# Kernel optimization log

Measured on AMD Instinct MI355X. Metric: run time of the kernel, lower is better.

Reference implementation:

```python
import jax, jax.numpy as jnp
import numpy as np

EPS_LN = 1e-6
EPS_NORM = 1e-7


def conv1x1(x, w, b):
    # x: [B,Cin,H,W], w: [Cout,Cin], b: [Cout]
    return jnp.einsum('bchw,oc->bohw', x, w) + b[None, :, None, None]


def ln2d(x, g, beta):
    u = x.mean(1, keepdims=True)
    s = ((x - u) ** 2).mean(1, keepdims=True)
    return g[None, :, None, None] * ((x - u) / jnp.sqrt(s + EPS_LN)) + beta[None, :, None, None]


def gather_neighborhoods(x, r):
    # x: [B,C,H,W] -> [B,C,n,H,W] with zero padding, n=(2r+1)**2
    B, C, H, W = x.shape
    xp = jnp.pad(x, ((0, 0), (0, 0), (r, r), (r, r)))
    slices = [xp[:, :, dy:dy + H, dx:dx + W]
              for dy in range(2 * r + 1) for dx in range(2 * r + 1)]
    return jnp.stack(slices, axis=2)


def valid_mask(H, W, r):
    offs = jnp.arange(-r, r + 1)
    hh = jnp.arange(H)
    ww = jnp.arange(W)
    vy = ((hh[None, :] + offs[:, None]) >= 0) & ((hh[None, :] + offs[:, None]) < H)  # [d,H]
    vx = ((ww[None, :] + offs[:, None]) >= 0) & ((ww[None, :] + offs[:, None]) < W)  # [d,W]
    return (vy[:, None, :, None] & vx[None, :, None, :]).reshape((2 * r + 1) ** 2, H, W)


def setup_inputs() -> dict:
    key = jax.random.key(0)
    B, C, H, W, r = 2, 64, 112, 112, 3
    n2 = (2 * r + 1) ** 2  # 49
    ks = jax.random.split(key, 16)
    s = 0.02
    inp = {
        'spatial_feats': jax.random.normal(ks[0], (B, C, H, W), jnp.float32),
        'semantic_feats': jax.random.normal(ks[1], (B, C, H, W), jnp.float32),
        # range_proj: conv1x1 -> LN2d -> SiLU -> conv1x1
        'rp_w1': s * jax.random.normal(ks[2], (C, C), jnp.float32), 'rp_b1': jnp.zeros((C,), jnp.float32),
        'rp_g': jnp.ones((C,), jnp.float32), 'rp_beta': jnp.zeros((C,), jnp.float32),
        'rp_w2': s * jax.random.normal(ks[3], (C, C), jnp.float32), 'rp_b2': jnp.zeros((C,), jnp.float32),
        # fixup_proj: conv1x1 (n2+C -> n2) -> LN2d -> SiLU -> conv1x1 (n2->n2)
        'fx_w1': s * jax.random.normal(ks[4], (n2, n2 + C), jnp.float32), 'fx_b1': jnp.zeros((n2,), jnp.float32),
        'fx_g': jnp.ones((n2,), jnp.float32), 'fx_beta': jnp.zeros((n2,), jnp.float32),
        'fx_w2': s * jax.random.normal(ks[5], (n2, n2), jnp.float32), 'fx_b2': jnp.zeros((n2,), jnp.float32),
        # output_proj: conv1x1 -> LN2d -> conv1x1
        'op_w1': s * jax.random.normal(ks[6], (C, C), jnp.float32), 'op_b1': jnp.zeros((C,), jnp.float32),
        'op_g': jnp.ones((C,), jnp.float32), 'op_beta': jnp.zeros((C,), jnp.float32),
        'op_w2': s * jax.random.normal(ks[7], (C, C), jnp.float32), 'op_b2': jnp.zeros((C,), jnp.float32),
        'sigma_spatial': jnp.array(1.0, jnp.float32),
    }
    return inp


def reference(spatial_feats, semantic_feats,
              rp_w1, rp_b1, rp_g, rp_beta, rp_w2, rp_b2,
              fx_w1, fx_b1, fx_g, fx_beta, fx_w2, fx_b2,
              op_w1, op_b1, op_g, op_beta, op_w2, op_b2,
              sigma_spatial):
    r = 3
    B, C, H, W = spatial_feats.shape
    # range_proj(semantic)
    px = conv1x1(semantic_feats, rp_w1, rp_b1)
    px = jax.nn.silu(ln2d(px, rp_g, rp_beta))
    px = conv1x1(px, rp_w2, rp_b2)

    # bilateral combined kernel: spatial Gaussian * range Gaussian, zero outside bounds
    offs = jnp.arange(-r, r + 1, dtype=jnp.float32)
    d2 = (offs[:, None] ** 2 + offs[None, :] ** 2).reshape(-1)  # [n2]
    sw = jnp.exp(-d2 / (2.0 * sigma_spatial ** 2))              # [n2]

    nbr = gather_neighborhoods(px, r)                            # [B,C,n2,H,W]
    nbr_sq = (nbr ** 2).sum(1)                                   # [B,n2,H,W]
    ctr_sq = (px ** 2).sum(1)                                    # [B,H,W]
    dot = jnp.einsum('bcnhw,bchw->bnhw', nbr, px)
    dist2 = jnp.maximum(nbr_sq + ctr_sq[:, None] - 2.0 * dot, 0.0)
    rw = jnp.exp(-dist2 / (2.0 * C))                             # range Gaussian, scale^2 = dim

    valid = valid_mask(H, W, r).astype(px.dtype)                 # [n2,H,W]
    combined = rw * sw[None, :, None, None] * valid[None]        # [B,n2,H,W]

    # gated fixup
    f = conv1x1(jnp.concatenate([combined, semantic_feats], axis=1), fx_w1, fx_b1)
    f = jax.nn.silu(ln2d(f, fx_g, fx_beta))
    f = conv1x1(f, fx_w2, fx_b2)
    combined = combined * (1.0 + jax.nn.sigmoid(f))
    combined = combined / (combined.sum(1, keepdims=True) + EPS_NORM)

    # neighborhood-weighted reduction of spatial feats
    nbhd = gather_neighborhoods(spatial_feats, r)                # [B,C,n2,H,W]
    out = jnp.einsum('bcnhw,bnhw->bchw', nbhd, combined)

    out = conv1x1(out, op_w1, op_b1)
    out = ln2d(out, op_g, op_beta)
    out = conv1x1(out, op_w2, op_b2)
    return out
```

## Files before the change

kernel.cpp:

```cpp
#include <hip/hip_runtime.h>

typedef unsigned short ushort;
typedef unsigned int uint;

constexpr int B = 2, C = 64, H = 112, W = 112;
constexpr int HW = H * W;
constexpr int NPIX = B * HW;
constexpr int NBLK = 512;
constexpr float EPS_LN = 1e-6f, EPS_NORM = 1e-7f;

typedef __attribute__((ext_vector_type(8))) short bf16x8;
typedef __attribute__((ext_vector_type(4))) float f32x4;

__device__ __forceinline__ float rcp_fast(float x) { return __builtin_amdgcn_rcpf(x); }
__device__ __forceinline__ float sigmoid_f(float x) { return rcp_fast(1.f + __expf(-x)); }
__device__ __forceinline__ int uni(int x) { return __builtin_amdgcn_readfirstlane(x); }
__device__ __forceinline__ int div7s(int x)  { return (x * 9363) >> 16; }
__device__ __forceinline__ int div13s(int x) { return (x * 5042) >> 16; }
__device__ __forceinline__ int div49s(int x) { return (x * 1338) >> 16; }

__device__ __forceinline__ ushort rne16(float x) {
    uint u = __float_as_uint(x);
    u += 0x7fffu + ((u >> 16) & 1u);
    return (ushort)(u >> 16);
}
__device__ __forceinline__ uint pack2(float a, float b) {
    return (uint)rne16(a) | ((uint)rne16(b) << 16);
}
__device__ __forceinline__ float2 up2(uint u) {
    return make_float2(__uint_as_float(u << 16), __uint_as_float(u & 0xffff0000u));
}

__device__ __forceinline__ f32x4 mfma16(bf16x8 a, bf16x8 b, f32x4 c) {
    return __builtin_amdgcn_mfma_f32_16x16x32_bf16(a, b, c, 0, 0, 0);
}

__device__ __forceinline__ void decode_blk(int blk, int& b, int& ty, int& tx) {
    int p8 = blk & 7, i = blk >> 3;
    b = p8 >> 2;
    int quad = p8 & 3;
    int lty = i >> 3, ltx = i & 7;
    ty = (quad >> 1) * 8 + lty;
    tx = (quad & 1) * 8 + ltx;
}

__device__ __forceinline__ void stage_w(const float* __restrict__ wsrc,
                                        ushort* wh, ushort* wl, int tid)
{
#pragma unroll
    for (int i = 0; i < 8; ++i) {
        int idx2 = i * 256 + tid;
        int o = idx2 >> 5, k = (idx2 & 31) * 2;
        float2 xy = *(const float2*)&wsrc[o * 64 + k];
        uint h = pack2(xy.x, xy.y);
        *(uint*)&wh[o * 72 + k] = h;
        *(uint*)&wl[o * 72 + k] = pack2(xy.x - __uint_as_float((h & 0xffffu) << 16),
                                        xy.y - __uint_as_float(h & 0xffff0000u));
    }
}

__device__ __forceinline__ void gemm64(const ushort* __restrict__ wh, const ushort* __restrict__ wl,
                                       const ushort* __restrict__ xh, const ushort* __restrict__ xl,
                                       const float* __restrict__ bias,
                                       int lm, int l4, int pp, f32x4 acc[4])
{
#pragma unroll
    for (int mt = 0; mt < 4; ++mt) {
        const int ob = mt * 16 + l4 * 4;
        acc[mt][0] = bias[ob]; acc[mt][1] = bias[ob + 1];
        acc[mt][2] = bias[ob + 2]; acc[mt][3] = bias[ob + 3];
    }
#pragma unroll
    for (int kt = 0; kt < 2; ++kt) {
        const int xo = pp * 72 + kt * 32 + l4 * 8;
        bf16x8 bh = *(const bf16x8*)&xh[xo];
        bf16x8 bl = *(const bf16x8*)&xl[xo];
#pragma unroll
        for (int mt = 0; mt < 4; ++mt) {
            const int wo = (mt * 16 + lm) * 72 + kt * 32 + l4 * 8;
            bf16x8 ah = *(const bf16x8*)&wh[wo];
            bf16x8 al = *(const bf16x8*)&wl[wo];
            acc[mt] = mfma16(al, bh, acc[mt]);
            acc[mt] = mfma16(ah, bl, acc[mt]);
            acc[mt] = mfma16(ah, bh, acc[mt]);
        }
    }
}

__global__ __launch_bounds__(256) void k1_range_proj(
    const float* __restrict__ sem,
    const float* __restrict__ w1, const float* __restrict__ b1,
    const float* __restrict__ g,  const float* __restrict__ be,
    const float* __restrict__ w2, const float* __restrict__ b2,
    ushort* __restrict__ px16, float* __restrict__ sqnorm)
{
    __shared__ __align__(16) ushort u16[28160];
    ushort* wh1 = u16;
    ushort* wl1 = u16 + 4608;
    ushort* wh2 = u16 + 9216;
    ushort* wl2 = u16 + 13824;
    ushort* xh  = u16 + 18432;
    ushort* xl  = u16 + 23040;
    float*  bv  = (float*)(u16 + 27648);

    const int tid = threadIdx.x, lane = tid & 63, wv = tid >> 6;
    const int lm = lane & 15, l4 = lane >> 4;
    int b, ty, tx; decode_blk(blockIdx.x, b, ty, tx);

    {
        const int lp = lane < 49 ? lane : 48;
        const int py = div7s(lp), px = lp - py * 7;
        const int hw = (ty * 7 + py) * W + tx * 7 + px;
        const bool a = lane < 49;
        float xv[16];
#pragma unroll
        for (int j = 0; j < 16; ++j)
            xv[j] = a ? sem[(size_t)(b * 64 + wv * 16 + j) * HW + hw] : 0.f;
        uint hu[8], lu[8];
#pragma unroll
        for (int jj = 0; jj < 8; ++jj) {
            uint hh = pack2(xv[2 * jj], xv[2 * jj + 1]);
            hu[jj] = hh;
            lu[jj] = pack2(xv[2 * jj]     - __uint_as_float((hh & 0xffffu) << 16),
                           xv[2 * jj + 1] - __uint_as_float(hh & 0xffff0000u));
        }
        const int rb = lane * 72 + wv * 16;
        *(uint4*)&xh[rb]     = make_uint4(hu[0], hu[1], hu[2], hu[3]);
        *(uint4*)&xh[rb + 8] = make_uint4(hu[4], hu[5], hu[6], hu[7]);
        *(uint4*)&xl[rb]     = make_uint4(lu[0], lu[1], lu[2], lu[3]);
        *(uint4*)&xl[rb + 8] = make_uint4(lu[4], lu[5], lu[6], lu[7]);
    }
    stage_w(w1, wh1, wl1, tid);
    stage_w(w2, wh2, wl2, tid);
    if (tid < 64) { bv[tid] = b1[tid]; bv[64 + tid] = g[tid];
                    bv[128 + tid] = be[tid]; bv[192 + tid] = b2[tid]; }
    __syncthreads();

    const int pp = wv * 16 + lm;
    f32x4 f[4];
    gemm64(wh1, wl1, xh, xl, bv, lm, l4, pp, f);

    float psum = 0.f, psq = 0.f;
#pragma unroll
    for (int mt = 0; mt < 4; ++mt)
#pragma unroll
        for (int r = 0; r < 4; ++r) { float fv = f[mt][r]; psum += fv; psq += fv * fv; }
    psum += __shfl_xor(psum, 16); psum += __shfl_xor(psum, 32);
    psq  += __shfl_xor(psq, 16);  psq  += __shfl_xor(psq, 32);
    const float m = psum * (1.f / 64.f);
    const float rstd = rsqrtf(psq * (1.f / 64.f) - m * m + EPS_LN);

    float sv_[16];
#pragma unroll
    for (int mt = 0; mt < 4; ++mt)
#pragma unroll
        for (int r = 0; r < 4; ++r) {
            const int o = mt * 16 + l4 * 4 + r;
            float y = bv[64 + o] * (f[mt][r] - m) * rstd + bv[128 + o];
            sv_[mt * 4 + r] = y * sigmoid_f(y);
        }
    __syncthreads();
#pragma unroll
    for (int mt = 0; mt < 4; ++mt) {
        uint h0 = pack2(sv_[4 * mt],     sv_[4 * mt + 1]);
        uint h1 = pack2(sv_[4 * mt + 2], sv_[4 * mt + 3]);
        uint l0 = pack2(sv_[4 * mt]     - __uint_as_float((h0 & 0xffffu) << 16),
                        sv_[4 * mt + 1] - __uint_as_float(h0 & 0xffff0000u));
        uint l1 = pack2(sv_[4 * mt + 2] - __uint_as_float((h1 & 0xffffu) << 16),
                        sv_[4 * mt + 3] - __uint_as_float(h1 & 0xffff0000u));
        const int so = pp * 72 + mt * 16 + l4 * 4;
        *(uint2*)&xh[so] = make_uint2(h0, h1);
        *(uint2*)&xl[so] = make_uint2(l0, l1);
    }
    __syncthreads();

    f32x4 z[4];
    gemm64(wh2, wl2, xh, xl, bv + 192, lm, l4, pp, z);

    float sq = 0.f;
#pragma unroll
    for (int mt = 0; mt < 4; ++mt)
#pragma unroll
        for (int r = 0; r < 4; ++r) sq += z[mt][r] * z[mt][r];
    sq += __shfl_xor(sq, 16); sq += __shfl_xor(sq, 32);

    if (pp < 49) {
        const int py = div7s(pp), px = pp - py * 7;
        const int hwi = (ty * 7 + py) * W + tx * 7 + px;
        ushort* dst = &px16[((size_t)b * HW + hwi) * 64];
#pragma unroll
        for (int mt = 0; mt < 4; ++mt)
            *(uint2*)&dst[mt * 16 + l4 * 4] =
                make_uint2(pack2(z[mt][0], z[mt][1]), pack2(z[mt][2], z[mt][3]));
        if (l4 == 0) sqnorm[(size_t)b * HW + hwi] = sq;
    }
}

__global__ __launch_bounds__(256, 2) void k23_fused(
    const ushort* __restrict__ px16, const float* __restrict__ sqnorm,
    const float* __restrict__ sem,  const float* __restrict__ spat,
    const float* __restrict__ fw1, const float* __restrict__ fb1,
    const float* __restrict__ fg,  const float* __restrict__ fbe,
    const float* __restrict__ fw2, const float* __restrict__ fb2,
    const float* __restrict__ w1, const float* __restrict__ b1,
    const float* __restrict__ g,  const float* __restrict__ be,
    const float* __restrict__ w2, const float* __restrict__ b2,
    const float* __restrict__ sigma_, float* __restrict__ out)
{
    __shared__ __align__(16) float smem[18048];
    ushort* haloA = (ushort*)smem;
    ushort* haloB = (ushort*)(smem + 5408);
    float*  comb  = smem + 10816;
    float*  fscr  = smem + 13952;
    float*  sqn_l = smem + 17088;
    float*  pm3   = smem + 17264;
    float*  ps3   = smem + 17520;
    float*  pt    = smem + 17776;
    float*  dmat  = smem + 5408;
    float*  fwc  = smem;
    float*  fw2l = smem + 2401;
    ushort* whiP = (ushort*)smem;
    ushort* wloP = (ushort*)smem + 4608;
    ushort* ahiP = (ushort*)(smem + 5408);
    ushort* aloP = (ushort*)(smem + 5408) + 4608;
    float*  bvP  = smem + 13952;

    const int tid = threadIdx.x, lane = tid & 63, wv = tid >> 6;
    const int lm = lane & 15, l4 = lane >> 4;
    int b, ty, tx; decode_blk(blockIdx.x, b, ty, tx);
    const int lp  = lane < 49 ? lane : 48;
    const int py  = div7s(lp), pxl = lp - py * 7;
    const int h = ty * 7 + py, w = tx * 7 + pxl;
    const int hw = h * W + w;
    const int h0 = ty * 7 - 3, w0 = tx * 7 - 3;
    const bool act = lane < 49;

    float sv[64];
#pragma unroll
    for (int k = 0; k < 64; ++k) sv[k] = sem[(size_t)(b * 64 + k) * HW + hw];

    for (int i = 0; i < 6; ++i) {
        int idx = i * 256 + tid;
        if (idx < 1352) {
            int r = idx >> 3, q = idx & 7;
            int ry = div13s(r), rx = r - ry * 13;
            int hh = h0 + ry, ww = w0 + rx;
            bool valid = (unsigned)hh < (unsigned)H && (unsigned)ww < (unsigned)W;
            uint4 v = make_uint4(0u, 0u, 0u, 0u);
            if (valid) v = *(const uint4*)&px16[((size_t)b * HW + hh * W + ww) * 64 + 8 * q];
            *(uint4*)&haloA[(r << 6) + ((q ^ (r & 7)) << 3)] = v;
        }
    }
    if (tid < 169) {
        int ry = div13s(tid), rx = tid - ry * 13;
        int hh = h0 + ry, ww = w0 + rx;
        bool valid = (unsigned)hh < (unsigned)H && (unsigned)ww < (unsigned)W;
        float v = 0.f;
        if (valid) v = sqnorm[(size_t)b * HW + hh * W + ww];
        sqn_l[tid] = v;
    }
    __syncthreads();

    {
        const int pp2 = wv * 16 + lm;
        const int qp = pp2 < 49 ? pp2 : 48;
        const int pyp = div7s(qp), pxp = qp - pyp * 7;
        const int rpp = pyp * 13 + pxp + 42;
        bf16x8 bc0 = *(const bf16x8*)&haloA[(rpp << 6) + ((l4 ^ (rpp & 7)) << 3)];
        bf16x8 bc1 = *(const bf16x8*)&haloA[(rpp << 6) + (((4 + l4) ^ (rpp & 7)) << 3)];
#pragma unroll
        for (int mt = 0; mt < 11; ++mt) {
            const int r = mt * 16 + lm;
            bf16x8 a0 = *(const bf16x8*)&haloA[(r << 6) + ((l4 ^ (r & 7)) << 3)];
            bf16x8 a1 = *(const bf16x8*)&haloA[(r << 6) + (((4 + l4) ^ (r & 7)) << 3)];
            f32x4 d = {0.f, 0.f, 0.f, 0.f};
            d = mfma16(a0, bc0, d);
            d = mfma16(a1, bc1, d);
            const int orow = mt * 16 + l4 * 4;
#pragma unroll
            for (int rr = 0; rr < 4; ++rr)
                dmat[(orow + rr) * 66 + pp2] = d[rr];
        }
    }
    __syncthreads();

    const int rbase = py * 13 + pxl;
    const int rp = rbase + 42;
    float cbl[13];
    {
        const float sqc = sqn_l[rp];
        const float sg_ = sigma_[0];
        const float inv2s2 = rcp_fast(2.f * sg_ * sg_);
#pragma unroll
        for (int i = 0; i < 13; ++i) {
            const int n = uni(wv + 4 * i);
            cbl[i] = 0.f;
            if (n < 49) {
                int ryn = div7s(n), rxn = n - ryn * 7;
                int dy = ryn - 3, dx = rxn - 3;
                int rn = rbase + ryn * 13 + rxn;
                float dot = dmat[rn * 66 + lane];
                float dist2 = fmaxf(sqn_l[rn] + sqc - 2.f * dot, 0.f);
                bool validn = (unsigned)(h + dy) < (unsigned)H && (unsigned)(w + dx) < (unsigned)W;
                float d2n = (float)(dy * dy + dx * dx);
                cbl[i] = validn ? __expf(-(dist2 * (1.f / 128.f) + d2n * inv2s2)) : 0.f;
            }
        }
    }
    for (int i = tid; i < 2401; i += 256) {
        int o = div49s(i);
        fwc[i]  = fw1[o * 113 + (i - o * 49)];
        fw2l[i] = fw2[i];
    }
    __syncthreads();

#pragma unroll
    for (int i = 0; i < 13; ++i) {
        const int n = wv + 4 * i;
        if (n < 49) comb[n * 64 + lane] = cbl[i];
    }
    if (tid < 169) {
        const int ry = div13s(tid), rx = tid - ry * 13;
        const int hh = h0 + ry, ww = w0 + rx;
        const bool valid = (unsigned)hh < (unsigned)H && (unsigned)ww < (unsigned)W;
        const int soff = hh * W + ww;
        const int rsw = (tid & 7), rb_ = tid << 6;
#pragma unroll
        for (int cq = 0; cq < 8; ++cq) {
            uint4 v = make_uint4(0u, 0u, 0u, 0u);
            if (valid) {
                const float* sp = &spat[(size_t)(b * 64 + 8 * cq) * HW + soff];
                v.x = pack2(sp[0],      sp[HW]);
                v.y = pack2(sp[2 * HW], sp[3 * HW]);
                v.z = pack2(sp[4 * HW], sp[5 * HW]);
                v.w = pack2(sp[6 * HW], sp[7 * HW]);
            }
            *(uint4*)&haloB[rb_ + ((cq ^ rsw) << 3)] = v;
        }
    }
    __syncthreads();

    float cb[49];
#pragma unroll
    for (int n = 0; n < 49; ++n) cb[n] = comb[n * 64 + lane];
    float macc = 0.f, sacc = 0.f;
    for (int i = 0; i < 13; ++i) {
        const int o = uni(wv + 4 * i);
        if (o < 49) {
            const float* wr = &fwc[o * 49];
            float a0 = 0, a1 = 0, a2 = 0, a3 = 0;
#pragma unroll
            for (int k = 0; k < 48; k += 4) {
                a0 += wr[k] * cb[k];       a1 += wr[k + 1] * cb[k + 1];
                a2 += wr[k + 2] * cb[k + 2]; a3 += wr[k + 3] * cb[k + 3];
            }
            a0 += wr[48] * cb[48];
            const float* wr2 = &fw1[o * 113 + 49];
#pragma unroll
            for (int k = 0; k < 64; k += 4) {
                a0 += wr2[k] * sv[k];       a1 += wr2[k + 1] * sv[k + 1];
                a2 += wr2[k + 2] * sv[k + 2]; a3 += wr2[k + 3] * sv[k + 3];
            }
            float f = (a0 + a1) + (a2 + a3) + fb1[o];
            fscr[o * 64 + lane] = f;
            macc += f; sacc += f * f;
        }
    }
    pm3[wv * 64 + lane] = macc; ps3[wv * 64 + lane] = sacc;
    __syncthreads();
    {
        float m  = (pm3[lane] + pm3[64 + lane] + pm3[128 + lane] + pm3[192 + lane]) * (1.f / 49.f);
        float va = (ps3[lane] + ps3[64 + lane] + ps3[128 + lane] + ps3[192 + lane]) * (1.f / 49.f) - m * m;
        float rstd = rsqrtf(va + EPS_LN);
        float s[49];
#pragma unroll
        for (int k = 0; k < 49; ++k) {
            float y = fg[k] * (fscr[k * 64 + lane] - m) * rstd + fbe[k];
            s[k] = y * sigmoid_f(y);
        }
        float tacc = 0.f;
        for (int i = 0; i < 13; ++i) {
            const int o = uni(wv + 4 * i);
            if (o < 49) {
                const float* wr = &fw2l[o * 49];
                float a0 = 0, a1 = 0, a2 = 0, a3 = 0;
#pragma unroll
                for (int k = 0; k < 48; k += 4) {
                    a0 += wr[k] * s[k];       a1 += wr[k + 1] * s[k + 1];
                    a2 += wr[k + 2] * s[k + 2]; a3 += wr[k + 3] * s[k + 3];
                }
                a0 += wr[48] * s[48];
                float fo = (a0 + a1) + (a2 + a3) + fb2[o];
                float gate = 1.f + sigmoid_f(fo);
                float cx = comb[o * 64 + lane] * gate;
                comb[o * 64 + lane] = cx;
                tacc += cx;
            }
        }
        pt[wv * 64 + lane] = tacc;
    }
    __syncthreads();
    const float inv = rcp_fast(pt[lane] + pt[64 + lane] + pt[128 + lane] + pt[192 + lane] + EPS_NORM);

    stage_w(w1, whiP, wloP, tid);
    if (tid < 64) { bvP[tid] = b1[tid]; bvP[64 + tid] = g[tid];
                    bvP[128 + tid] = be[tid]; bvP[192 + tid] = b2[tid]; }

    const int c0 = uni(wv * 16);
    const int qq0 = c0 >> 3;
    float acc[16];
#pragma unroll
    for (int j = 0; j < 16; ++j) acc[j] = 0.f;
    for (int n = 0; n < 49; ++n) {
        int ryn = n / 7, rxn = n - ryn * 7;
        int rn = rbase + ryn * 13 + rxn;
        float cn = comb[n * 64 + lane] * inv;
        const int rb_ = rn << 6, rsw = rn & 7;
#pragma unroll
        for (int q = 0; q < 2; ++q) {
            uint4 v = *(const uint4*)&haloB[rb_ + (((qq0 + q) ^ rsw) << 3)];
            float2 a = up2(v.x), bb = up2(v.y), c = up2(v.z), d = up2(v.w);
            acc[8 * q + 0] += cn * a.x;  acc[8 * q + 1] += cn * a.y;
            acc[8 * q + 2] += cn * bb.x; acc[8 * q + 3] += cn * bb.y;
            acc[8 * q + 4] += cn * c.x;  acc[8 * q + 5] += cn * c.y;
            acc[8 * q + 6] += cn * d.x;  acc[8 * q + 7] += cn * d.y;
        }
    }
    __syncthreads();

    {
        uint hu[8], lu[8];
#pragma unroll
        for (int jj = 0; jj < 8; ++jj) {
            float x0 = act ? acc[2 * jj] : 0.f;
            float x1 = act ? acc[2 * jj + 1] : 0.f;
            uint hh = pack2(x0, x1);
            hu[jj] = hh;
            lu[jj] = pack2(x0 - __uint_as_float((hh & 0xffffu) << 16),
                           x1 - __uint_as_float(hh & 0xffff0000u));
        }
        const int rb = lane * 72 + c0;
        *(uint4*)&ahiP[rb]     = make_uint4(hu[0], hu[1], hu[2], hu[3]);
        *(uint4*)&ahiP[rb + 8] = make_uint4(hu[4], hu[5], hu[6], hu[7]);
        *(uint4*)&aloP[rb]     = make_uint4(lu[0], lu[1], lu[2], lu[3]);
        *(uint4*)&aloP[rb + 8] = make_uint4(lu[4], lu[5], lu[6], lu[7]);
    }
    __syncthreads();

    const int pp = wv * 16 + lm;
    f32x4 f6[4];
    gemm64(whiP, wloP, ahiP, aloP, bvP, lm, l4, pp, f6);

    float psum = 0.f, psq = 0.f;
#pragma unroll
    for (int mt = 0; mt < 4; ++mt)
#pragma unroll
        for (int r = 0; r < 4; ++r) { float fv = f6[mt][r]; psum += fv; psq += fv * fv; }
    psum += __shfl_xor(psum, 16); psum += __shfl_xor(psum, 32);
    psq  += __shfl_xor(psq, 16);  psq  += __shfl_xor(psq, 32);
    const float m6 = psum * (1.f / 64.f);
    const float rstd6 = rsqrtf(psq * (1.f / 64.f) - m6 * m6 + EPS_LN);

    float yv[16];
#pragma unroll
    for (int mt = 0; mt < 4; ++mt)
#pragma unroll
        for (int r = 0; r < 4; ++r) {
            const int o = mt * 16 + l4 * 4 + r;
            yv[mt * 4 + r] = bvP[64 + o] * (f6[mt][r] - m6) * rstd6 + bvP[128 + o];
        }
    __syncthreads();

#pragma unroll
    for (int mt = 0; mt < 4; ++mt) {
        uint h0 = pack2(yv[4 * mt],     yv[4 * mt + 1]);
        uint h1 = pack2(yv[4 * mt + 2], yv[4 * mt + 3]);
        uint l0 = pack2(yv[4 * mt]     - __uint_as_float((h0 & 0xffffu) << 16),
                        yv[4 * mt + 1] - __uint_as_float(h0 & 0xffff0000u));
        uint l1 = pack2(yv[4 * mt + 2] - __uint_as_float((h1 & 0xffffu) << 16),
                        yv[4 * mt + 3] - __uint_as_float(h1 & 0xffff0000u));
        const int so = pp * 72 + mt * 16 + l4 * 4;
        *(uint2*)&ahiP[so] = make_uint2(h0, h1);
        *(uint2*)&aloP[so] = make_uint2(l0, l1);
    }
    stage_w(w2, whiP, wloP, tid);
    __syncthreads();

    f32x4 z6[4];
    gemm64(whiP, wloP, ahiP, aloP, bvP + 192, lm, l4, pp, z6);

    if (pp < 49) {
        const int py6 = div7s(pp), px6 = pp - py6 * 7;
        const int hwi6 = (ty * 7 + py6) * W + tx * 7 + px6;
#pragma unroll
        for (int mt = 0; mt < 4; ++mt)
#pragma unroll
            for (int r = 0; r < 4; ++r)
                out[(size_t)(b * 64 + mt * 16 + l4 * 4 + r) * HW + hwi6] = z6[mt][r];
    }
}

extern "C" void kernel_launch(void* const* d_in, const int* in_sizes, int n_in,
                              void* d_out, int out_size, void* d_ws, size_t ws_size,
                              hipStream_t stream)
{
    const float* spatial  = (const float*)d_in[0];
    const float* semantic = (const float*)d_in[1];
    const float* rp_w1 = (const float*)d_in[2];
    const float* rp_b1 = (const float*)d_in[3];
    const float* rp_g  = (const float*)d_in[4];
    const float* rp_be = (const float*)d_in[5];
    const float* rp_w2 = (const float*)d_in[6];
    const float* rp_b2 = (const float*)d_in[7];
    const float* fx_w1 = (const float*)d_in[8];
    const float* fx_b1 = (const float*)d_in[9];
    const float* fx_g  = (const float*)d_in[10];
    const float* fx_be = (const float*)d_in[11];
    const float* fx_w2 = (const float*)d_in[12];
    const float* fx_b2 = (const float*)d_in[13];
    const float* op_w1 = (const float*)d_in[14];
    const float* op_b1 = (const float*)d_in[15];
    const float* op_g  = (const float*)d_in[16];
    const float* op_be = (const float*)d_in[17];
    const float* op_w2 = (const float*)d_in[18];
    const float* op_b2 = (const float*)d_in[19];
    const float* sigma = (const float*)d_in[20];

    ushort* px16  = (ushort*)d_ws;
    float* sqnorm = (float*)((char*)d_ws + (size_t)NPIX * 64 * 2);

    k1_range_proj<<<NBLK, 256, 0, stream>>>(
        semantic, rp_w1, rp_b1, rp_g, rp_be, rp_w2, rp_b2, px16, sqnorm);
    k23_fused<<<NBLK, 256, 0, stream>>>(
        px16, sqnorm, semantic, spatial,
        fx_w1, fx_b1, fx_g, fx_be, fx_w2, fx_b2,
        op_w1, op_b1, op_g, op_be, op_w2, op_b2,
        sigma, (float*)d_out);
}
```

Before: 155.8 us.

## Fuse range projection into main kernel with recomputed 13x13 halo

Removes the separate range-projection kernel and its global px16/sqnorm intermediates. Each block now recomputes the two-layer range projection (conv, LN, SiLU, conv) for its full 13x13 halo (169 pixels) directly into shared memory, then builds the swizzled halo and squared norms from registers. This saves one launch and the global round trip, at the cost of roughly 3.4x redundant GEMM work per tile, a re-laid-out shared memory map, and extra register pressure from holding packed results.

```diff
diff --git a/kernel.cpp b/kernel.cpp
--- a/kernel.cpp
+++ b/kernel.cpp
@@ -5,7 +5,6 @@
 
 constexpr int B = 2, C = 64, H = 112, W = 112;
 constexpr int HW = H * W;
-constexpr int NPIX = B * HW;
 constexpr int NBLK = 512;
 constexpr float EPS_LN = 1e-6f, EPS_NORM = 1e-7f;
 
@@ -87,118 +86,11 @@
     }
 }
 
-__global__ __launch_bounds__(256) void k1_range_proj(
-    const float* __restrict__ sem,
-    const float* __restrict__ w1, const float* __restrict__ b1,
-    const float* __restrict__ g,  const float* __restrict__ be,
-    const float* __restrict__ w2, const float* __restrict__ b2,
-    ushort* __restrict__ px16, float* __restrict__ sqnorm)
-{
-    __shared__ __align__(16) ushort u16[28160];
-    ushort* wh1 = u16;
-    ushort* wl1 = u16 + 4608;
-    ushort* wh2 = u16 + 9216;
-    ushort* wl2 = u16 + 13824;
-    ushort* xh  = u16 + 18432;
-    ushort* xl  = u16 + 23040;
-    float*  bv  = (float*)(u16 + 27648);
-
-    const int tid = threadIdx.x, lane = tid & 63, wv = tid >> 6;
-    const int lm = lane & 15, l4 = lane >> 4;
-    int b, ty, tx; decode_blk(blockIdx.x, b, ty, tx);
-
-    {
-        const int lp = lane < 49 ? lane : 48;
-        const int py = div7s(lp), px = lp - py * 7;
-        const int hw = (ty * 7 + py) * W + tx * 7 + px;
-        const bool a = lane < 49;
-        float xv[16];
-#pragma unroll
-        for (int j = 0; j < 16; ++j)
-            xv[j] = a ? sem[(size_t)(b * 64 + wv * 16 + j) * HW + hw] : 0.f;
-        uint hu[8], lu[8];
-#pragma unroll
-        for (int jj = 0; jj < 8; ++jj) {
-            uint hh = pack2(xv[2 * jj], xv[2 * jj + 1]);
-            hu[jj] = hh;
-            lu[jj] = pack2(xv[2 * jj]     - __uint_as_float((hh & 0xffffu) << 16),
-                           xv[2 * jj + 1] - __uint_as_float(hh & 0xffff0000u));
-        }
-        const int rb = lane * 72 + wv * 16;
-        *(uint4*)&xh[rb]     = make_uint4(hu[0], hu[1], hu[2], hu[3]);
-        *(uint4*)&xh[rb + 8] = make_uint4(hu[4], hu[5], hu[6], hu[7]);
-        *(uint4*)&xl[rb]     = make_uint4(lu[0], lu[1], lu[2], lu[3]);
-        *(uint4*)&xl[rb + 8] = make_uint4(lu[4], lu[5], lu[6], lu[7]);
-    }
-    stage_w(w1, wh1, wl1, tid);
-    stage_w(w2, wh2, wl2, tid);
-    if (tid < 64) { bv[tid] = b1[tid]; bv[64 + tid] = g[tid];
-                    bv[128 + tid] = be[tid]; bv[192 + tid] = b2[tid]; }
-    __syncthreads();
-
-    const int pp = wv * 16 + lm;
-    f32x4 f[4];
-    gemm64(wh1, wl1, xh, xl, bv, lm, l4, pp, f);
-
-    float psum = 0.f, psq = 0.f;
-#pragma unroll
-    for (int mt = 0; mt < 4; ++mt)
-#pragma unroll
-        for (int r = 0; r < 4; ++r) { float fv = f[mt][r]; psum += fv; psq += fv * fv; }
-    psum += __shfl_xor(psum, 16); psum += __shfl_xor(psum, 32);
-    psq  += __shfl_xor(psq, 16);  psq  += __shfl_xor(psq, 32);
-    const float m = psum * (1.f / 64.f);
-    const float rstd = rsqrtf(psq * (1.f / 64.f) - m * m + EPS_LN);
-
-    float sv_[16];
-#pragma unroll
-    for (int mt = 0; mt < 4; ++mt)
-#pragma unroll
-        for (int r = 0; r < 4; ++r) {
-            const int o = mt * 16 + l4 * 4 + r;
-            float y = bv[64 + o] * (f[mt][r] - m) * rstd + bv[128 + o];
-            sv_[mt * 4 + r] = y * sigmoid_f(y);
-        }
-    __syncthreads();
-#pragma unroll
-    for (int mt = 0; mt < 4; ++mt) {
-        uint h0 = pack2(sv_[4 * mt],     sv_[4 * mt + 1]);
-        uint h1 = pack2(sv_[4 * mt + 2], sv_[4 * mt + 3]);
-        uint l0 = pack2(sv_[4 * mt]     - __uint_as_float((h0 & 0xffffu) << 16),
-                        sv_[4 * mt + 1] - __uint_as_float(h0 & 0xffff0000u));
-        uint l1 = pack2(sv_[4 * mt + 2] - __uint_as_float((h1 & 0xffffu) << 16),
-                        sv_[4 * mt + 3] - __uint_as_float(h1 & 0xffff0000u));
-        const int so = pp * 72 + mt * 16 + l4 * 4;
-        *(uint2*)&xh[so] = make_uint2(h0, h1);
-        *(uint2*)&xl[so] = make_uint2(l0, l1);
-    }
-    __syncthreads();
-
-    f32x4 z[4];
-    gemm64(wh2, wl2, xh, xl, bv + 192, lm, l4, pp, z);
-
-    float sq = 0.f;
-#pragma unroll
-    for (int mt = 0; mt < 4; ++mt)
-#pragma unroll
-        for (int r = 0; r < 4; ++r) sq += z[mt][r] * z[mt][r];
-    sq += __shfl_xor(sq, 16); sq += __shfl_xor(sq, 32);
-
-    if (pp < 49) {
-        const int py = div7s(pp), px = pp - py * 7;
-        const int hwi = (ty * 7 + py) * W + tx * 7 + px;
-        ushort* dst = &px16[((size_t)b * HW + hwi) * 64];
-#pragma unroll
-        for (int mt = 0; mt < 4; ++mt)
-            *(uint2*)&dst[mt * 16 + l4 * 4] =
-                make_uint2(pack2(z[mt][0], z[mt][1]), pack2(z[mt][2], z[mt][3]));
-        if (l4 == 0) sqnorm[(size_t)b * HW + hwi] = sq;
-    }
-}
-
-__global__ __launch_bounds__(256, 2) void k23_fused(
-    const ushort* __restrict__ px16, const float* __restrict__ sqnorm,
+__global__ __launch_bounds__(256, 2) void k_fused(
     const float* __restrict__ sem,  const float* __restrict__ spat,
+    const float* __restrict__ rw1, const float* __restrict__ rb1,
+    const float* __restrict__ rg,  const float* __restrict__ rbe,
+    const float* __restrict__ rw2, const float* __restrict__ rb2,
     const float* __restrict__ fw1, const float* __restrict__ fb1,
     const float* __restrict__ fg,  const float* __restrict__ fbe,
     const float* __restrict__ fw2, const float* __restrict__ fb2,
@@ -207,23 +99,28 @@
     const float* __restrict__ w2, const float* __restrict__ b2,
     const float* __restrict__ sigma_, float* __restrict__ out)
 {
-    __shared__ __align__(16) float smem[18048];
+    __shared__ __align__(16) float smem[17536];
+    ushort* whA = (ushort*)smem;
+    ushort* wlA = (ushort*)smem + 4608;
+    ushort* xhA = (ushort*)(smem + 4608);
+    ushort* xlA = (ushort*)(smem + 4608) + 12672;
+    float*  bvA = smem + 17280;
     ushort* haloA = (ushort*)smem;
-    ushort* haloB = (ushort*)(smem + 5408);
-    float*  comb  = smem + 10816;
-    float*  fscr  = smem + 13952;
-    float*  sqn_l = smem + 17088;
-    float*  pm3   = smem + 17264;
-    float*  ps3   = smem + 17520;
-    float*  pt    = smem + 17776;
-    float*  dmat  = smem + 5408;
-    float*  fwc  = smem;
-    float*  fw2l = smem + 2401;
+    float*  sqn_l = smem + 5408;
+    float*  dmat  = smem + 5616;
+    float*  fwc   = smem;
+    float*  fw2l  = smem + 2401;
+    float*  comb  = smem + 4802;
+    ushort* haloB = (ushort*)(smem + 7938);
+    float*  fscr  = smem + 13346;
+    float*  pm3   = smem + 16482;
+    float*  ps3   = smem + 16738;
+    float*  pt    = smem + 16994;
     ushort* whiP = (ushort*)smem;
     ushort* wloP = (ushort*)smem + 4608;
-    ushort* ahiP = (ushort*)(smem + 5408);
-    ushort* aloP = (ushort*)(smem + 5408) + 4608;
-    float*  bvP  = smem + 13952;
+    float*  bvP  = smem + 16482;
+    ushort* ahiP = (ushort*)(smem + 4802);
+    ushort* aloP = (ushort*)(smem + 4802) + 4608;
 
     const int tid = threadIdx.x, lane = tid & 63, wv = tid >> 6;
     const int lm = lane & 15, l4 = lane >> 4;
@@ -234,36 +131,135 @@
     const int hw = h * W + w;
     const int h0 = ty * 7 - 3, w0 = tx * 7 - 3;
     const bool act = lane < 49;
-
-    float sv[64];
-#pragma unroll
-    for (int k = 0; k < 64; ++k) sv[k] = sem[(size_t)(b * 64 + k) * HW + hw];
-
-    for (int i = 0; i < 6; ++i) {
-        int idx = i * 256 + tid;
-        if (idx < 1352) {
-            int r = idx >> 3, q = idx & 7;
+    const int pp = wv * 16 + lm;
+
+    if (tid < 176) {
+        const int r = tid;
+        bool valid = false; int soff = 0;
+        if (r < 169) {
             int ry = div13s(r), rx = r - ry * 13;
             int hh = h0 + ry, ww = w0 + rx;
+            valid = (unsigned)hh < (unsigned)H && (unsigned)ww < (unsigned)W;
+            soff = hh * W + ww;
+        }
+#pragma unroll
+        for (int cq = 0; cq < 8; ++cq) {
+            float x[8];
+#pragma unroll
+            for (int j = 0; j < 8; ++j)
+                x[j] = valid ? sem[(size_t)(b * 64 + cq * 8 + j) * HW + soff] : 0.f;
+            uint hu[4], lu[4];
+#pragma unroll
+            for (int j = 0; j < 4; ++j) {
+                uint hh2 = pack2(x[2 * j], x[2 * j + 1]);
+                hu[j] = hh2;
+                lu[j] = pack2(x[2 * j]     - __uint_as_float((hh2 & 0xffffu) << 16),
+                              x[2 * j + 1] - __uint_as_float(hh2 & 0xffff0000u));
+            }
+            *(uint4*)&xhA[r * 72 + cq * 8] = make_uint4(hu[0], hu[1], hu[2], hu[3]);
+            *(uint4*)&xlA[r * 72 + cq * 8] = make_uint4(lu[0], lu[1], lu[2], lu[3]);
+        }
+    }
+    stage_w(rw1, whA, wlA, tid);
+    if (tid < 64) { bvA[tid] = rb1[tid]; bvA[64 + tid] = rg[tid];
+                    bvA[128 + tid] = rbe[tid]; bvA[192 + tid] = rb2[tid]; }
+    __syncthreads();
+
+#pragma unroll
+    for (int i = 0; i < 3; ++i) {
+        const int nt = wv + 4 * i;
+        if (nt < 11) {
+            const int p = nt * 16 + lm;
+            f32x4 f1[4];
+            gemm64(whA, wlA, xhA, xlA, bvA, lm, l4, p, f1);
+            float psum = 0.f, psq = 0.f;
+#pragma unroll
+            for (int mt = 0; mt < 4; ++mt)
+#pragma unroll
+                for (int r = 0; r < 4; ++r) { float fv = f1[mt][r]; psum += fv; psq += fv * fv; }
+            psum += __shfl_xor(psum, 16); psum += __shfl_xor(psum, 32);
+            psq  += __shfl_xor(psq, 16);  psq  += __shfl_xor(psq, 32);
+            const float m = psum * (1.f / 64.f);
+            const float rstd = rsqrtf(psq * (1.f / 64.f) - m * m + EPS_LN);
+#pragma unroll
+            for (int mt = 0; mt < 4; ++mt) {
+                float s0, s1, s2, s3;
+                {
+                    const int o = mt * 16 + l4 * 4;
+                    float y0 = bvA[64 + o]     * (f1[mt][0] - m) * rstd + bvA[128 + o];
+                    float y1 = bvA[64 + o + 1] * (f1[mt][1] - m) * rstd + bvA[128 + o + 1];
+                    float y2 = bvA[64 + o + 2] * (f1[mt][2] - m) * rstd + bvA[128 + o + 2];
+                    float y3 = bvA[64 + o + 3] * (f1[mt][3] - m) * rstd + bvA[128 + o + 3];
+                    s0 = y0 * sigmoid_f(y0); s1 = y1 * sigmoid_f(y1);
+                    s2 = y2 * sigmoid_f(y2); s3 = y3 * sigmoid_f(y3);
+                }
+                uint h0_ = pack2(s0, s1), h1_ = pack2(s2, s3);
+                uint l0_ = pack2(s0 - __uint_as_float((h0_ & 0xffffu) << 16),
+                                 s1 - __uint_as_float(h0_ & 0xffff0000u));
+                uint l1_ = pack2(s2 - __uint_as_float((h1_ & 0xffffu) << 16),
+                                 s3 - __uint_as_float(h1_ & 0xffff0000u));
+                const int so = p * 72 + mt * 16 + l4 * 4;
+                *(uint2*)&xhA[so] = make_uint2(h0_, h1_);
+                *(uint2*)&xlA[so] = make_uint2(l0_, l1_);
+            }
+        }
+    }
+    __syncthreads();
+    stage_w(rw2, whA, wlA, tid);
+    __syncthreads();
+
+    uint zpk[24];
+    float sqs[3];
+#pragma unroll
+    for (int i = 0; i < 3; ++i) {
+        const int nt = wv + 4 * i;
+        if (nt < 11) {
+            const int p = nt * 16 + lm;
+            f32x4 z1[4];
+            gemm64(whA, wlA, xhA, xlA, bvA + 192, lm, l4, p, z1);
+            float sq = 0.f;
+#pragma unroll
+            for (int mt = 0; mt < 4; ++mt)
+#pragma unroll
+                for (int r = 0; r < 4; ++r) sq += z1[mt][r] * z1[mt][r];
+            sq += __shfl_xor(sq, 16); sq += __shfl_xor(sq, 32);
+            sqs[i] = sq;
+#pragma unroll
+            for (int mt = 0; mt < 4; ++mt) {
+                zpk[i * 8 + 2 * mt]     = pack2(z1[mt][0], z1[mt][1]);
+                zpk[i * 8 + 2 * mt + 1] = pack2(z1[mt][2], z1[mt][3]);
+            }
+        }
+    }
+    __syncthreads();
+
+#pragma unroll
+    for (int i = 0; i < 3; ++i) {
+        const int nt = wv + 4 * i;
+        const int p = nt * 16 + lm;
+        if (nt < 11 && p < 169) {
+            int ry = div13s(p), rx = p - ry * 13;
+            int hh = h0 + ry, ww = w0 + rx;
             bool valid = (unsigned)hh < (unsigned)H && (unsigned)ww < (unsigned)W;
-            uint4 v = make_uint4(0u, 0u, 0u, 0u);
-            if (valid) v = *(const uint4*)&px16[((size_t)b * HW + hh * W + ww) * 64 + 8 * q];
-            *(uint4*)&haloA[(r << 6) + ((q ^ (r & 7)) << 3)] = v;
-        }
-    }
-    if (tid < 169) {
-        int ry = div13s(tid), rx = tid - ry * 13;
-        int hh = h0 + ry, ww = w0 + rx;
-        bool valid = (unsigned)hh < (unsigned)H && (unsigned)ww < (unsigned)W;
-        float v = 0.f;
-        if (valid) v = sqnorm[(size_t)b * HW + hh * W + ww];
-        sqn_l[tid] = v;
-    }
+#pragma unroll
+            for (int mt = 0; mt < 4; ++mt) {
+                const int ch = mt * 16 + l4 * 4;
+                const int q8 = ch >> 3;
+                const int off = (p << 6) + ((q8 ^ (p & 7)) << 3) + (ch & 7);
+                uint2 v = valid ? make_uint2(zpk[i * 8 + 2 * mt], zpk[i * 8 + 2 * mt + 1])
+                                : make_uint2(0u, 0u);
+                *(uint2*)&haloA[off] = v;
+            }
+            if (l4 == 0) sqn_l[p] = valid ? sqs[i] : 0.f;
+        }
+    }
+    float sv[64];
+#pragma unroll
+    for (int k = 0; k < 64; ++k) sv[k] = sem[(size_t)(b * 64 + k) * HW + hw];
     __syncthreads();
 
     {
-        const int pp2 = wv * 16 + lm;
-        const int qp = pp2 < 49 ? pp2 : 48;
+        const int qp = pp < 49 ? pp : 48;
         const int pyp = div7s(qp), pxp = qp - pyp * 7;
         const int rpp = pyp * 13 + pxp + 42;
         bf16x8 bc0 = *(const bf16x8*)&haloA[(rpp << 6) + ((l4 ^ (rpp & 7)) << 3)];
@@ -279,7 +275,7 @@
             const int orow = mt * 16 + l4 * 4;
 #pragma unroll
             for (int rr = 0; rr < 4; ++rr)
-                dmat[(orow + rr) * 66 + pp2] = d[rr];
+                dmat[(orow + rr) * 66 + pp] = d[rr];
         }
     }
     __syncthreads();
@@ -340,33 +336,35 @@
     }
     __syncthreads();
 
-    float cb[49];
-#pragma unroll
-    for (int n = 0; n < 49; ++n) cb[n] = comb[n * 64 + lane];
-    float macc = 0.f, sacc = 0.f;
-    for (int i = 0; i < 13; ++i) {
-        const int o = uni(wv + 4 * i);
-        if (o < 49) {
-            const float* wr = &fwc[o * 49];
-            float a0 = 0, a1 = 0, a2 = 0, a3 = 0;
-#pragma unroll
-            for (int k = 0; k < 48; k += 4) {
-                a0 += wr[k] * cb[k];       a1 += wr[k + 1] * cb[k + 1];
-                a2 += wr[k + 2] * cb[k + 2]; a3 += wr[k + 3] * cb[k + 3];
-            }
-            a0 += wr[48] * cb[48];
-            const float* wr2 = &fw1[o * 113 + 49];
-#pragma unroll
-            for (int k = 0; k < 64; k += 4) {
-                a0 += wr2[k] * sv[k];       a1 += wr2[k + 1] * sv[k + 1];
-                a2 += wr2[k + 2] * sv[k + 2]; a3 += wr2[k + 3] * sv[k + 3];
-            }
-            float f = (a0 + a1) + (a2 + a3) + fb1[o];
-            fscr[o * 64 + lane] = f;
-            macc += f; sacc += f * f;
-        }
-    }
-    pm3[wv * 64 + lane] = macc; ps3[wv * 64 + lane] = sacc;
+    {
+        float cb[49];
+#pragma unroll
+        for (int n = 0; n < 49; ++n) cb[n] = comb[n * 64 + lane];
+        float macc = 0.f, sacc = 0.f;
+        for (int i = 0; i < 13; ++i) {
+            const int o = uni(wv + 4 * i);
+            if (o < 49) {
+                const float* wr = &fwc[o * 49];
+                float a0 = 0, a1 = 0, a2 = 0, a3 = 0;
+#pragma unroll
+                for (int k = 0; k < 48; k += 4) {
+                    a0 += wr[k] * cb[k];       a1 += wr[k + 1] * cb[k + 1];
+                    a2 += wr[k + 2] * cb[k + 2]; a3 += wr[k + 3] * cb[k + 3];
+                }
+                a0 += wr[48] * cb[48];
+                const float* wr2 = &fw1[o * 113 + 49];
+#pragma unroll
+                for (int k = 0; k < 64; k += 4) {
+                    a0 += wr2[k] * sv[k];       a1 += wr2[k + 1] * sv[k + 1];
+                    a2 += wr2[k + 2] * sv[k + 2]; a3 += wr2[k + 3] * sv[k + 3];
+                }
+                float f = (a0 + a1) + (a2 + a3) + fb1[o];
+                fscr[o * 64 + lane] = f;
+                macc += f; sacc += f * f;
+            }
+        }
+        pm3[wv * 64 + lane] = macc; ps3[wv * 64 + lane] = sacc;
+    }
     __syncthreads();
     {
         float m  = (pm3[lane] + pm3[64 + lane] + pm3[128 + lane] + pm3[192 + lane]) * (1.f / 49.f);
@@ -447,7 +445,6 @@
     }
     __syncthreads();
 
-    const int pp = wv * 16 + lm;
     f32x4 f6[4];
     gemm64(whiP, wloP, ahiP, aloP, bvP, lm, l4, pp, f6);
 
@@ -473,15 +470,15 @@
 
 #pragma unroll
     for (int mt = 0; mt < 4; ++mt) {
-        uint h0 = pack2(yv[4 * mt],     yv[4 * mt + 1]);
-        uint h1 = pack2(yv[4 * mt + 2], yv[4 * mt + 3]);
-        uint l0 = pack2(yv[4 * mt]     - __uint_as_float((h0 & 0xffffu) << 16),
-                        yv[4 * mt + 1] - __uint_as_float(h0 & 0xffff0000u));
-        uint l1 = pack2(yv[4 * mt + 2] - __uint_as_float((h1 & 0xffffu) << 16),
-                        yv[4 * mt + 3] - __uint_as_float(h1 & 0xffff0000u));
+        uint h0_ = pack2(yv[4 * mt],     yv[4 * mt + 1]);
+        uint h1_ = pack2(yv[4 * mt + 2], yv[4 * mt + 3]);
+        uint l0_ = pack2(yv[4 * mt]     - __uint_as_float((h0_ & 0xffffu) << 16),
+                         yv[4 * mt + 1] - __uint_as_float(h0_ & 0xffff0000u));
+        uint l1_ = pack2(yv[4 * mt + 2] - __uint_as_float((h1_ & 0xffffu) << 16),
+                         yv[4 * mt + 3] - __uint_as_float(h1_ & 0xffff0000u));
         const int so = pp * 72 + mt * 16 + l4 * 4;
-        *(uint2*)&ahiP[so] = make_uint2(h0, h1);
-        *(uint2*)&aloP[so] = make_uint2(l0, l1);
+        *(uint2*)&ahiP[so] = make_uint2(h0_, h1_);
+        *(uint2*)&aloP[so] = make_uint2(l0_, l1_);
     }
     stage_w(w2, whiP, wloP, tid);
     __syncthreads();
@@ -526,13 +523,9 @@
     const float* op_b2 = (const float*)d_in[19];
     const float* sigma = (const float*)d_in[20];
 
-    ushort* px16  = (ushort*)d_ws;
-    float* sqnorm = (float*)((char*)d_ws + (size_t)NPIX * 64 * 2);
-
-    k1_range_proj<<<NBLK, 256, 0, stream>>>(
-        semantic, rp_w1, rp_b1, rp_g, rp_be, rp_w2, rp_b2, px16, sqnorm);
-    k23_fused<<<NBLK, 256, 0, stream>>>(
-        px16, sqnorm, semantic, spatial,
+    k_fused<<<NBLK, 256, 0, stream>>>(
+        semantic, spatial,
+        rp_w1, rp_b1, rp_g, rp_be, rp_w2, rp_b2,
         fx_w1, fx_b1, fx_g, fx_be, fx_w2, fx_b2,
         op_w1, op_b1, op_g, op_be, op_w2, op_b2,
         sigma, (float*)d_out);
```

New measurement: 176.2 us. 1.13x slower.

## Move fixup projection convs onto split-bf16 MFMA with repacked shared memory

Applied to the files above, without the earlier changes.

The gated-fixup MLP (two 1x1 convs with LayerNorm and SiLU) moves from scalar FMA loops over per-lane register arrays onto MFMA 16x16x32 bf16 using a hi/lo three-product split, padding the 49 channels to 64. The shared-memory layout is reorganised to hold the padded weight and activation tiles. The LayerNorm and normalisation reductions now use cross-lane shuffles instead of shared-memory partial sums. This adds several barriers and padding work on 15 unused channels, and it changes numerical precision slightly through the split-bf16 approximation.

```diff
diff --git a/kernel.cpp b/kernel.cpp
--- a/kernel.cpp
+++ b/kernel.cpp
@@ -17,7 +17,6 @@
 __device__ __forceinline__ int uni(int x) { return __builtin_amdgcn_readfirstlane(x); }
 __device__ __forceinline__ int div7s(int x)  { return (x * 9363) >> 16; }
 __device__ __forceinline__ int div13s(int x) { return (x * 5042) >> 16; }
-__device__ __forceinline__ int div49s(int x) { return (x * 1338) >> 16; }
 
 __device__ __forceinline__ ushort rne16(float x) {
     uint u = __float_as_uint(x);
@@ -29,6 +28,9 @@
 }
 __device__ __forceinline__ float2 up2(uint u) {
     return make_float2(__uint_as_float(u << 16), __uint_as_float(u & 0xffff0000u));
+}
+__device__ __forceinline__ float up1(ushort u) {
+    return __uint_as_float((uint)u << 16);
 }
 
 __device__ __forceinline__ f32x4 mfma16(bf16x8 a, bf16x8 b, f32x4 c) {
@@ -59,17 +61,28 @@
     }
 }
 
-__device__ __forceinline__ void gemm64(const ushort* __restrict__ wh, const ushort* __restrict__ wl,
-                                       const ushort* __restrict__ xh, const ushort* __restrict__ xl,
-                                       const float* __restrict__ bias,
-                                       int lm, int l4, int pp, f32x4 acc[4])
+__device__ __forceinline__ void stage_wpad(const float* __restrict__ src, int ld,
+                                           int nrow, int ncol,
+                                           ushort* wh, ushort* wl, int tid)
 {
-#pragma unroll
-    for (int mt = 0; mt < 4; ++mt) {
-        const int ob = mt * 16 + l4 * 4;
-        acc[mt][0] = bias[ob]; acc[mt][1] = bias[ob + 1];
-        acc[mt][2] = bias[ob + 2]; acc[mt][3] = bias[ob + 3];
-    }
+    const int o = tid >> 2, q = (tid & 3) * 16;
+#pragma unroll
+    for (int jj = 0; jj < 8; ++jj) {
+        int c = q + 2 * jj;
+        float x0 = (o < nrow && c < ncol)     ? src[o * ld + c]     : 0.f;
+        float x1 = (o < nrow && c + 1 < ncol) ? src[o * ld + c + 1] : 0.f;
+        uint hh = pack2(x0, x1);
+        uint ll = pack2(x0 - __uint_as_float((hh & 0xffffu) << 16),
+                        x1 - __uint_as_float(hh & 0xffff0000u));
+        *(uint*)&wh[o * 72 + c] = hh;
+        *(uint*)&wl[o * 72 + c] = ll;
+    }
+}
+
+__device__ __forceinline__ void gemm64_acc(const ushort* __restrict__ wh, const ushort* __restrict__ wl,
+                                           const ushort* __restrict__ xh, const ushort* __restrict__ xl,
+                                           int lm, int l4, int pp, f32x4 acc[4])
+{
 #pragma unroll
     for (int kt = 0; kt < 2; ++kt) {
         const int xo = pp * 72 + kt * 32 + l4 * 8;
@@ -85,6 +98,20 @@
             acc[mt] = mfma16(ah, bh, acc[mt]);
         }
     }
+}
+
+__device__ __forceinline__ void gemm64(const ushort* __restrict__ wh, const ushort* __restrict__ wl,
+                                       const ushort* __restrict__ xh, const ushort* __restrict__ xl,
+                                       const float* __restrict__ bias,
+                                       int lm, int l4, int pp, f32x4 acc[4])
+{
+#pragma unroll
+    for (int mt = 0; mt < 4; ++mt) {
+        const int ob = mt * 16 + l4 * 4;
+        acc[mt][0] = bias[ob]; acc[mt][1] = bias[ob + 1];
+        acc[mt][2] = bias[ob + 2]; acc[mt][3] = bias[ob + 3];
+    }
+    gemm64_acc(wh, wl, xh, xl, lm, l4, pp, acc);
 }
 
 __global__ __launch_bounds__(256) void k1_range_proj(
@@ -209,21 +236,21 @@
 {
     __shared__ __align__(16) float smem[18048];
     ushort* haloA = (ushort*)smem;
-    ushort* haloB = (ushort*)(smem + 5408);
-    float*  comb  = smem + 10816;
-    float*  fscr  = smem + 13952;
+    float*  dmat  = smem + 5408;
     float*  sqn_l = smem + 17088;
-    float*  pm3   = smem + 17264;
-    float*  ps3   = smem + 17520;
-    float*  pt    = smem + 17776;
-    float*  dmat  = smem + 5408;
-    float*  fwc  = smem;
-    float*  fw2l = smem + 2401;
-    ushort* whiP = (ushort*)smem;
-    ushort* wloP = (ushort*)smem + 4608;
-    ushort* ahiP = (ushort*)(smem + 5408);
-    ushort* aloP = (ushort*)(smem + 5408) + 4608;
-    float*  bvP  = smem + 13952;
+    float*  comb  = smem;
+    float*  bv3   = smem + 3136;
+    float*  pt    = smem + 3136;
+    ushort* Xh    = (ushort*)(smem + 3392);
+    ushort* Xl    = (ushort*)(smem + 5696);
+    ushort* Ah    = (ushort*)(smem + 8000);
+    ushort* Al    = (ushort*)(smem + 10304);
+    ushort* haloB = (ushort*)(smem + 12640);
+    float*  bvP   = smem + 3136;
+    ushort* whiP  = (ushort*)(smem + 8000);
+    ushort* wloP  = (ushort*)(smem + 10304);
+    ushort* ahiP  = (ushort*)(smem + 3392);
+    ushort* aloP  = (ushort*)(smem + 5696);
 
     const int tid = threadIdx.x, lane = tid & 63, wv = tid >> 6;
     const int lm = lane & 15, l4 = lane >> 4;
@@ -234,6 +261,7 @@
     const int hw = h * W + w;
     const int h0 = ty * 7 - 3, w0 = tx * 7 - 3;
     const bool act = lane < 49;
+    const int pp = wv * 16 + lm;
 
     float sv[64];
 #pragma unroll
@@ -262,8 +290,7 @@
     __syncthreads();
 
     {
-        const int pp2 = wv * 16 + lm;
-        const int qp = pp2 < 49 ? pp2 : 48;
+        const int qp = pp < 49 ? pp : 48;
         const int pyp = div7s(qp), pxp = qp - pyp * 7;
         const int rpp = pyp * 13 + pxp + 42;
         bf16x8 bc0 = *(const bf16x8*)&haloA[(rpp << 6) + ((l4 ^ (rpp & 7)) << 3)];
@@ -279,7 +306,7 @@
             const int orow = mt * 16 + l4 * 4;
 #pragma unroll
             for (int rr = 0; rr < 4; ++rr)
-                dmat[(orow + rr) * 66 + pp2] = d[rr];
+                dmat[(orow + rr) * 66 + pp] = d[rr];
         }
     }
     __syncthreads();
@@ -307,17 +334,26 @@
             }
         }
     }
-    for (int i = tid; i < 2401; i += 256) {
-        int o = div49s(i);
-        fwc[i]  = fw1[o * 113 + (i - o * 49)];
-        fw2l[i] = fw2[i];
-    }
     __syncthreads();
 
 #pragma unroll
     for (int i = 0; i < 13; ++i) {
         const int n = wv + 4 * i;
-        if (n < 49) comb[n * 64 + lane] = cbl[i];
+        if (n < 49) {
+            float v = cbl[i];
+            comb[n * 64 + lane] = v;
+            ushort hh = rne16(v);
+            Xh[lane * 72 + n] = hh;
+            Xl[lane * 72 + n] = rne16(v - up1(hh));
+        }
+    }
+    if (tid < 64) {
+#pragma unroll
+        for (int r = 49; r < 64; ++r) { Xh[tid * 72 + r] = 0; Xl[tid * 72 + r] = 0; }
+        bv3[tid]       = (tid < 49) ? fb1[tid] : 0.f;
+        bv3[64 + tid]  = (tid < 49) ? fb2[tid] : 0.f;
+        bv3[128 + tid] = (tid < 49) ? fg[tid]  : 0.f;
+        bv3[192 + tid] = (tid < 49) ? fbe[tid] : 0.f;
     }
     if (tid < 169) {
         const int ry = div13s(tid), rx = tid - ry * 13;
@@ -338,69 +374,101 @@
             *(uint4*)&haloB[rb_ + ((cq ^ rsw) << 3)] = v;
         }
     }
-    __syncthreads();
-
-    float cb[49];
-#pragma unroll
-    for (int n = 0; n < 49; ++n) cb[n] = comb[n * 64 + lane];
-    float macc = 0.f, sacc = 0.f;
-    for (int i = 0; i < 13; ++i) {
-        const int o = uni(wv + 4 * i);
-        if (o < 49) {
-            const float* wr = &fwc[o * 49];
-            float a0 = 0, a1 = 0, a2 = 0, a3 = 0;
-#pragma unroll
-            for (int k = 0; k < 48; k += 4) {
-                a0 += wr[k] * cb[k];       a1 += wr[k + 1] * cb[k + 1];
-                a2 += wr[k + 2] * cb[k + 2]; a3 += wr[k + 3] * cb[k + 3];
+    stage_wpad(fw1, 113, 49, 49, Ah, Al, tid);
+    __syncthreads();
+
+    f32x4 accF[4];
+    gemm64(Ah, Al, Xh, Xl, bv3, lm, l4, pp, accF);
+    __syncthreads();
+
+    {
+        uint hu[8], lu[8];
+#pragma unroll
+        for (int jj = 0; jj < 8; ++jj) {
+            float x0 = sv[wv * 16 + 2 * jj], x1 = sv[wv * 16 + 2 * jj + 1];
+            uint hh = pack2(x0, x1);
+            hu[jj] = hh;
+            lu[jj] = pack2(x0 - __uint_as_float((hh & 0xffffu) << 16),
+                           x1 - __uint_as_float(hh & 0xffff0000u));
+        }
+        const int rb = lane * 72 + wv * 16;
+        *(uint4*)&Xh[rb]     = make_uint4(hu[0], hu[1], hu[2], hu[3]);
+        *(uint4*)&Xh[rb + 8] = make_uint4(hu[4], hu[5], hu[6], hu[7]);
+        *(uint4*)&Xl[rb]     = make_uint4(lu[0], lu[1], lu[2], lu[3]);
+        *(uint4*)&Xl[rb + 8] = make_uint4(lu[4], lu[5], lu[6], lu[7]);
+    }
+    stage_wpad(fw1 + 49, 113, 49, 64, Ah, Al, tid);
+    __syncthreads();
+
+    gemm64_acc(Ah, Al, Xh, Xl, lm, l4, pp, accF);
+
+    float sarr[16];
+    {
+        float psum = 0.f, psq = 0.f;
+#pragma unroll
+        for (int mt = 0; mt < 4; ++mt)
+#pragma unroll
+            for (int r = 0; r < 4; ++r) {
+                const int o = mt * 16 + l4 * 4 + r;
+                if (o < 49) { float fv = accF[mt][r]; psum += fv; psq += fv * fv; }
             }
-            a0 += wr[48] * cb[48];
-            const float* wr2 = &fw1[o * 113 + 49];
-#pragma unroll
-            for (int k = 0; k < 64; k += 4) {
-                a0 += wr2[k] * sv[k];       a1 += wr2[k + 1] * sv[k + 1];
-                a2 += wr2[k + 2] * sv[k + 2]; a3 += wr2[k + 3] * sv[k + 3];
+        psum += __shfl_xor(psum, 16); psum += __shfl_xor(psum, 32);
+        psq  += __shfl_xor(psq, 16);  psq  += __shfl_xor(psq, 32);
+        const float m = psum * (1.f / 49.f);
+        const float rstd = rsqrtf(psq * (1.f / 49.f) - m * m + EPS_LN);
+#pragma unroll
+        for (int mt = 0; mt < 4; ++mt)
+#pragma unroll
+            for (int r = 0; r < 4; ++r) {
+                const int o = mt * 16 + l4 * 4 + r;
+                float s = 0.f;
+                if (o < 49) {
+                    float y = bv3[128 + o] * (accF[mt][r] - m) * rstd + bv3[192 + o];
+                    s = y * sigmoid_f(y);
+                }
+                sarr[mt * 4 + r] = s;
             }
-            float f = (a0 + a1) + (a2 + a3) + fb1[o];
-            fscr[o * 64 + lane] = f;
-            macc += f; sacc += f * f;
-        }
-    }
-    pm3[wv * 64 + lane] = macc; ps3[wv * 64 + lane] = sacc;
-    __syncthreads();
+    }
+    __syncthreads();
+
+#pragma unroll
+    for (int mt = 0; mt < 4; ++mt) {
+        uint h0_ = pack2(sarr[4 * mt],     sarr[4 * mt + 1]);
+        uint h1_ = pack2(sarr[4 * mt + 2], sarr[4 * mt + 3]);
+        uint l0_ = pack2(sarr[4 * mt]     - __uint_as_float((h0_ & 0xffffu) << 16),
+                         sarr[4 * mt + 1] - __uint_as_float(h0_ & 0xffff0000u));
+        uint l1_ = pack2(sarr[4 * mt + 2] - __uint_as_float((h1_ & 0xffffu) << 16),
+                         sarr[4 * mt + 3] - __uint_as_float(h1_ & 0xffff0000u));
+        const int so = pp * 72 + mt * 16 + l4 * 4;
+        *(uint2*)&Xh[so] = make_uint2(h0_, h1_);
+        *(uint2*)&Xl[so] = make_uint2(l0_, l1_);
+    }
+    stage_wpad(fw2, 49, 49, 49, Ah, Al, tid);
+    __syncthreads();
+
+    f32x4 accG[4];
+    gemm64(Ah, Al, Xh, Xl, bv3 + 64, lm, l4, pp, accG);
+
     {
-        float m  = (pm3[lane] + pm3[64 + lane] + pm3[128 + lane] + pm3[192 + lane]) * (1.f / 49.f);
-        float va = (ps3[lane] + ps3[64 + lane] + ps3[128 + lane] + ps3[192 + lane]) * (1.f / 49.f) - m * m;
-        float rstd = rsqrtf(va + EPS_LN);
-        float s[49];
-#pragma unroll
-        for (int k = 0; k < 49; ++k) {
-            float y = fg[k] * (fscr[k * 64 + lane] - m) * rstd + fbe[k];
-            s[k] = y * sigmoid_f(y);
-        }
         float tacc = 0.f;
-        for (int i = 0; i < 13; ++i) {
-            const int o = uni(wv + 4 * i);
-            if (o < 49) {
-                const float* wr = &fw2l[o * 49];
-                float a0 = 0, a1 = 0, a2 = 0, a3 = 0;
-#pragma unroll
-                for (int k = 0; k < 48; k += 4) {
-                    a0 += wr[k] * s[k];       a1 += wr[k + 1] * s[k + 1];
-                    a2 += wr[k + 2] * s[k + 2]; a3 += wr[k + 3] * s[k + 3];
+#pragma unroll
+        for (int mt = 0; mt < 4; ++mt)
+#pragma unroll
+            for (int r = 0; r < 4; ++r) {
+                const int o = mt * 16 + l4 * 4 + r;
+                if (o < 49) {
+                    float gate = 1.f + sigmoid_f(accG[mt][r]);
+                    float cx = comb[o * 64 + pp] * gate;
+                    comb[o * 64 + pp] = cx;
+                    tacc += cx;
                 }
-                a0 += wr[48] * s[48];
-                float fo = (a0 + a1) + (a2 + a3) + fb2[o];
-                float gate = 1.f + sigmoid_f(fo);
-                float cx = comb[o * 64 + lane] * gate;
-                comb[o * 64 + lane] = cx;
-                tacc += cx;
             }
-        }
-        pt[wv * 64 + lane] = tacc;
-    }
-    __syncthreads();
-    const float inv = rcp_fast(pt[lane] + pt[64 + lane] + pt[128 + lane] + pt[192 + lane] + EPS_NORM);
+        tacc += __shfl_xor(tacc, 16); tacc += __shfl_xor(tacc, 32);
+        if (l4 == 0) pt[pp] = tacc;
+    }
+    __syncthreads();
+    const float inv = rcp_fast(pt[lane] + EPS_NORM);
+    __syncthreads();
 
     stage_w(w1, whiP, wloP, tid);
     if (tid < 64) { bvP[tid] = b1[tid]; bvP[64 + tid] = g[tid];
@@ -447,7 +515,6 @@
     }
     __syncthreads();
 
-    const int pp = wv * 16 + lm;
     f32x4 f6[4];
     gemm64(whiP, wloP, ahiP, aloP, bvP, lm, l4, pp, f6);
 
@@ -473,15 +540,15 @@
 
 #pragma unroll
     for (int mt = 0; mt < 4; ++mt) {
-        uint h0 = pack2(yv[4 * mt],     yv[4 * mt + 1]);
-        uint h1 = pack2(yv[4 * mt + 2], yv[4 * mt + 3]);
-        uint l0 = pack2(yv[4 * mt]     - __uint_as_float((h0 & 0xffffu) << 16),
-                        yv[4 * mt + 1] - __uint_as_float(h0 & 0xffff0000u));
-        uint l1 = pack2(yv[4 * mt + 2] - __uint_as_float((h1 & 0xffffu) << 16),
-                        yv[4 * mt + 3] - __uint_as_float(h1 & 0xffff0000u));
+        uint h0_ = pack2(yv[4 * mt],     yv[4 * mt + 1]);
+        uint h1_ = pack2(yv[4 * mt + 2], yv[4 * mt + 3]);
+        uint l0_ = pack2(yv[4 * mt]     - __uint_as_float((h0_ & 0xffffu) << 16),
+                         yv[4 * mt + 1] - __uint_as_float(h0_ & 0xffff0000u));
+        uint l1_ = pack2(yv[4 * mt + 2] - __uint_as_float((h1_ & 0xffffu) << 16),
+                         yv[4 * mt + 3] - __uint_as_float(h1_ & 0xffff0000u));
         const int so = pp * 72 + mt * 16 + l4 * 4;
-        *(uint2*)&ahiP[so] = make_uint2(h0, h1);
-        *(uint2*)&aloP[so] = make_uint2(l0, l1);
+        *(uint2*)&ahiP[so] = make_uint2(h0_, h1_);
+        *(uint2*)&aloP[so] = make_uint2(l0_, l1_);
     }
     stage_w(w2, whiP, wloP, tid);
     __syncthreads();
```

After: 152.2 us. 1.02x faster.
